# Kernel tuning notes

Hardware: AMD Instinct MI355X
Metric: run time of the kernel (lower is better)

Reference implementation:

```python
import jax, jax.numpy as jnp
import numpy as np

DIM = 128
N_ENT = 500000
N_REL = 500
GAMMA = 12.0
EPS = 1e-12  # F.normalize eps


def l2norm(x):
    n = jnp.sqrt(jnp.sum(x * x, axis=-1, keepdims=True))
    return x / jnp.maximum(n, EPS)


def setup_inputs() -> dict:
    key = jax.random.key(0)
    k1, k2, k3, k4, k5, k6 = jax.random.split(key, 6)
    B = 16384
    h = jax.random.randint(k1, (B,), 0, N_ENT)
    r = jax.random.randint(k2, (B,), 0, 2 * N_REL)
    t = jax.random.randint(k3, (B,), 0, N_ENT)
    # xavier_uniform-like init
    def xav(k, shape):
        bound = float(np.sqrt(6.0 / (shape[0] + shape[1])))
        return jax.random.uniform(k, shape, jnp.float32, -bound, bound)
    ent_w = xav(k4, (N_ENT, DIM))
    rel_w = xav(k5, (N_REL, DIM))
    mat_w = xav(k6, (N_REL, DIM * DIM))
    return {"h": h, "r": r, "t": t, "ent_w": ent_w, "rel_w": rel_w, "mat_w": mat_w}


def reference(h, r, t, ent_w, rel_w, mat_w):
    # r indexes into doubled tables: [mat; mat] and [rel; -rel]
    mat_full = jnp.concatenate([mat_w, mat_w], axis=0)          # [2R, D*D]
    rel_full = jnp.concatenate([rel_w, -rel_w], axis=0)         # [2R, D]
    mat = mat_full[r].reshape(-1, DIM, DIM)                      # [B, D, D]
    rv = l2norm(rel_full[r])                                     # [B, D]
    hv = l2norm(ent_w[h])                                        # [B, D]
    tv = l2norm(ent_w[t])                                        # [B, D]
    # _transfer: (1,D) @ (D,D) -> (D,), then L2 normalize
    hp = l2norm(jnp.einsum('bd,bde->be', hv, mat))
    tp = l2norm(jnp.einsum('bd,bde->be', tv, mat))
    dist = hp + rv - tp
    score = GAMMA - jnp.sqrt(jnp.sum(dist * dist, axis=-1))      # p=2 norm
    return score
```

## Files before the change

kernel.cpp:

```cpp
#include <hip/hip_runtime.h>

#define DIM   128
#define N_REL 500
#define GAMMA 12.0f
#define EPS   1e-12f


__global__ void k_zero(int* __restrict__ counts) {
    counts[threadIdx.x] = 0;
}

__global__ void k_hist(const int* __restrict__ r, int* __restrict__ counts, int B) {
    int i = blockIdx.x * 256 + threadIdx.x;
    if (i < B) {
        int ri = r[i];
        int mi = (ri >= N_REL) ? ri - N_REL : ri;
        atomicAdd(&counts[mi], 1);
    }
}

__global__ void k_scan(const int* __restrict__ counts,
                       int* __restrict__ offsets, int* __restrict__ cursor) {
    __shared__ int s[512];
    int tid = threadIdx.x;
    int v = counts[tid];
    s[tid] = v;
    __syncthreads();
    for (int off = 1; off < 512; off <<= 1) {
        int x = (tid >= off) ? s[tid - off] : 0;
        __syncthreads();
        s[tid] += x;
        __syncthreads();
    }
    int excl = s[tid] - v;
    offsets[tid] = excl;
    cursor[tid]  = excl;
}

__global__ void k_scatter(const int* __restrict__ r, int* __restrict__ cursor,
                          int* __restrict__ order, int B) {
    int i = blockIdx.x * 256 + threadIdx.x;
    if (i < B) {
        int ri = r[i];
        int mi = (ri >= N_REL) ? ri - N_REL : ri;
        int pos = atomicAdd(&cursor[mi], 1);
        order[pos] = i;
    }
}


__global__ __launch_bounds__(256) void k_matvec(
    const int* __restrict__ order, const int* __restrict__ offsets,
    const int* __restrict__ counts,
    const int* __restrict__ h, const int* __restrict__ t,
    const float* __restrict__ ent_w, const float* __restrict__ mat_w,
    float* __restrict__ hp_raw, float* __restrict__ tp_raw)
{
    const int rel = blockIdx.x;
    const int cnt_all = counts[rel];
    if (cnt_all == 0) return;
    const int start0 = offsets[rel];
    const int tid = threadIdx.x;
    const int eg = tid & 31;
    const int dc = tid >> 5;
    const int e128 = tid & 127;

    const float4* __restrict__ M4 = (const float4*)(mat_w + (size_t)rel * DIM * DIM);
    float4 Mreg[16];
#pragma unroll
    for (int dd = 0; dd < 16; ++dd)
        Mreg[dd] = M4[(dc * 16 + dd) * 32 + eg];

    __shared__ float sv[2][2][DIM];
    __shared__ float part[2][8][DIM];
    __shared__ int   sb[128], shi[128], sti[128];

    for (int chunk = 0; chunk < cnt_all; chunk += 128) {
        const int cc = min(128, cnt_all - chunk);

        if (tid < cc) {
            int b = order[start0 + chunk + tid];
            sb[tid]  = b;
            shi[tid] = h[b];
            sti[tid] = t[b];
        }
        __syncthreads();

        {
            int row = (tid < 128) ? shi[0] : sti[0];
            sv[0][tid >> 7][e128] = ent_w[(size_t)row * DIM + e128];
        }
        __syncthreads();

        for (int s = 0; s < cc; ++s) {
            const int cur = s & 1, nxt = cur ^ 1;

            float pre = 0.0f;
            if (s + 1 < cc) {
                int row = (tid < 128) ? shi[s + 1] : sti[s + 1];
                pre = ent_w[(size_t)row * DIM + e128];
            }

            float4 ah = make_float4(0.f, 0.f, 0.f, 0.f);
            float4 at = make_float4(0.f, 0.f, 0.f, 0.f);
#pragma unroll
            for (int dd = 0; dd < 16; ++dd) {
                const float  a = sv[cur][0][dc * 16 + dd];
                const float  c = sv[cur][1][dc * 16 + dd];
                const float4 m = Mreg[dd];
                ah.x += a * m.x; ah.y += a * m.y; ah.z += a * m.z; ah.w += a * m.w;
                at.x += c * m.x; at.y += c * m.y; at.z += c * m.z; at.w += c * m.w;
            }
            *(float4*)&part[0][dc][4 * eg] = ah;
            *(float4*)&part[1][dc][4 * eg] = at;
            __syncthreads();

            {
                const int b = sb[s];
                float v = 0.f;
                const int half = tid >> 7;
#pragma unroll
                for (int k = 0; k < 8; ++k) v += part[half][k][e128];
                float* dst = half ? tp_raw : hp_raw;
                dst[(size_t)b * DIM + e128] = v;
            }

            if (s + 1 < cc)
                sv[nxt][tid >> 7][e128] = pre;
            __syncthreads();
        }
    }
}


__device__ __forceinline__ float waveSum(float v) {
#pragma unroll
    for (int off = 32; off > 0; off >>= 1)
        v += __shfl_xor(v, off, 64);
    return v;
}

__global__ __launch_bounds__(256) void k_score(
    const int* __restrict__ r, const float* __restrict__ rel_w,
    const float* __restrict__ hp_raw, const float* __restrict__ tp_raw,
    float* __restrict__ out, int B)
{
    const int w    = threadIdx.x >> 6;
    const int lane = threadIdx.x & 63;
    const int b    = blockIdx.x * 4 + w;
    if (b >= B) return;

    const int   ri   = r[b];
    const int   mi   = (ri >= N_REL) ? ri - N_REL : ri;
    const float sign = (ri >= N_REL) ? -1.0f : 1.0f;

    const float2 hp = ((const float2*)(hp_raw + (size_t)b * DIM))[lane];
    const float2 tp = ((const float2*)(tp_raw + (size_t)b * DIM))[lane];
    const float2 rv = ((const float2*)(rel_w  + (size_t)mi * DIM))[lane];

    const float hs = waveSum(hp.x * hp.x + hp.y * hp.y);
    const float ts = waveSum(tp.x * tp.x + tp.y * tp.y);
    const float rs = waveSum(rv.x * rv.x + rv.y * rv.y);

    const float hinv = 1.0f / fmaxf(sqrtf(hs), EPS);
    const float tinv = 1.0f / fmaxf(sqrtf(ts), EPS);
    const float rinv = sign / fmaxf(sqrtf(rs), EPS);

    const float dx = hp.x * hinv + rv.x * rinv - tp.x * tinv;
    const float dy = hp.y * hinv + rv.y * rinv - tp.y * tinv;
    const float ds = waveSum(dx * dx + dy * dy);

    if (lane == 0) out[b] = GAMMA - sqrtf(ds);
}


extern "C" void kernel_launch(void* const* d_in, const int* in_sizes, int n_in,
                              void* d_out, int out_size, void* d_ws, size_t ws_size,
                              hipStream_t stream) {
    const int*   h     = (const int*)d_in[0];
    const int*   r     = (const int*)d_in[1];
    const int*   t     = (const int*)d_in[2];
    const float* ent_w = (const float*)d_in[3];
    const float* rel_w = (const float*)d_in[4];
    const float* mat_w = (const float*)d_in[5];
    float*       out   = (float*)d_out;
    const int B = in_sizes[0];

    int* counts  = (int*)d_ws;
    int* offsets = counts + 512;
    int* cursor  = counts + 1024;
    int* order   = counts + 1536;
    float* hp_raw = (float*)((char*)d_ws + (128 << 10));
    float* tp_raw = hp_raw + (size_t)B * DIM;

    k_zero   <<<1, 512, 0, stream>>>(counts);
    k_hist   <<<(B + 255) / 256, 256, 0, stream>>>(r, counts, B);
    k_scan   <<<1, 512, 0, stream>>>(counts, offsets, cursor);
    k_scatter<<<(B + 255) / 256, 256, 0, stream>>>(r, cursor, order, B);
    k_matvec <<<N_REL, 256, 0, stream>>>(order, offsets, counts, h, t,
                                         ent_w, mat_w, hp_raw, tp_raw);
    k_score  <<<(B + 3) / 4, 256, 0, stream>>>(r, rel_w, hp_raw, tp_raw, out, B);
}
```

Baseline: 367.6 us.

## Fuse scoring into matvec, merge bucketing kernels, split relations across blocks

Replaces the four bucketing kernels with one single-block kernel using shared-memory atomics and scan. It fuses the normalization and distance scoring into the matvec kernel, so the hp/tp intermediates no longer go to global memory. It also splits each relation's samples across four blocks to shorten the serial per-block loop and raise occupancy. The cost is reloading each relation matrix four times and adding an extra barrier per sample.

Result: slower. 384.4 us (+4.6%).

```diff
diff --git a/kernel.cpp b/kernel.cpp
--- a/kernel.cpp
+++ b/kernel.cpp
@@ -4,66 +4,82 @@
 #define N_REL 500
 #define GAMMA 12.0f
 #define EPS   1e-12f
+#define SPLIT 4
 
-
-__global__ void k_zero(int* __restrict__ counts) {
-    counts[threadIdx.x] = 0;
+__device__ __forceinline__ float waveSum(float v) {
+#pragma unroll
+    for (int off = 32; off > 0; off >>= 1)
+        v += __shfl_xor(v, off, 64);
+    return v;
 }
 
-__global__ void k_hist(const int* __restrict__ r, int* __restrict__ counts, int B) {
-    int i = blockIdx.x * 256 + threadIdx.x;
-    if (i < B) {
+__global__ __launch_bounds__(1024) void k_bucket(
+    const int* __restrict__ r, int B,
+    int* __restrict__ counts_g, int* __restrict__ offsets_g, int* __restrict__ order)
+{
+    __shared__ int sc[512];
+    __shared__ int sa[512];
+    __shared__ int scur[512];
+    const int tid = threadIdx.x;
+
+    if (tid < 512) sc[tid] = 0;
+    __syncthreads();
+
+    for (int i = tid; i < B; i += 1024) {
         int ri = r[i];
         int mi = (ri >= N_REL) ? ri - N_REL : ri;
-        atomicAdd(&counts[mi], 1);
+        atomicAdd(&sc[mi], 1);
     }
-}
+    __syncthreads();
 
-__global__ void k_scan(const int* __restrict__ counts,
-                       int* __restrict__ offsets, int* __restrict__ cursor) {
-    __shared__ int s[512];
-    int tid = threadIdx.x;
-    int v = counts[tid];
-    s[tid] = v;
+    if (tid < 512) sa[tid] = sc[tid];
     __syncthreads();
     for (int off = 1; off < 512; off <<= 1) {
-        int x = (tid >= off) ? s[tid - off] : 0;
+        int x = 0;
+        if (tid < 512) x = sa[tid] + ((tid >= off) ? sa[tid - off] : 0);
         __syncthreads();
-        s[tid] += x;
+        if (tid < 512) sa[tid] = x;
         __syncthreads();
     }
-    int excl = s[tid] - v;
-    offsets[tid] = excl;
-    cursor[tid]  = excl;
-}
+    if (tid < 512) {
+        int excl = sa[tid] - sc[tid];
+        offsets_g[tid] = excl;
+        counts_g[tid]  = sc[tid];
+        scur[tid]      = excl;
+    }
+    __syncthreads();
 
-__global__ void k_scatter(const int* __restrict__ r, int* __restrict__ cursor,
-                          int* __restrict__ order, int B) {
-    int i = blockIdx.x * 256 + threadIdx.x;
-    if (i < B) {
+    for (int i = tid; i < B; i += 1024) {
         int ri = r[i];
         int mi = (ri >= N_REL) ? ri - N_REL : ri;
-        int pos = atomicAdd(&cursor[mi], 1);
+        int pos = atomicAdd(&scur[mi], 1);
         order[pos] = i;
     }
 }
 
+__global__ __launch_bounds__(256) void k_main(
+    const int* __restrict__ order, const int* __restrict__ offsets_g,
+    const int* __restrict__ counts_g,
+    const int* __restrict__ h, const int* __restrict__ t, const int* __restrict__ r,
+    const float* __restrict__ ent_w, const float* __restrict__ rel_w,
+    const float* __restrict__ mat_w, float* __restrict__ out)
+{
+    const int rel = blockIdx.x / SPLIT;
+    const int sp  = blockIdx.x % SPLIT;
+    const int cnt = counts_g[rel];
+    const int lo  = (cnt * sp) / SPLIT;
+    const int hi  = (cnt * (sp + 1)) / SPLIT;
+    const int n   = hi - lo;
+    if (n <= 0) return;
+    const int base = offsets_g[rel] + lo;
 
-__global__ __launch_bounds__(256) void k_matvec(
-    const int* __restrict__ order, const int* __restrict__ offsets,
-    const int* __restrict__ counts,
-    const int* __restrict__ h, const int* __restrict__ t,
-    const float* __restrict__ ent_w, const float* __restrict__ mat_w,
-    float* __restrict__ hp_raw, float* __restrict__ tp_raw)
-{
-    const int rel = blockIdx.x;
-    const int cnt_all = counts[rel];
-    if (cnt_all == 0) return;
-    const int start0 = offsets[rel];
-    const int tid = threadIdx.x;
-    const int eg = tid & 31;
-    const int dc = tid >> 5;
-    const int e128 = tid & 127;
+    const int tid  = threadIdx.x;
+    const int eg   = tid & 31;
+    const int dc   = tid >> 5;
+    const int e    = tid & 127;
+    const int half = tid >> 7;
+    const int lane = tid & 63;
+    const int wv   = tid >> 6;
 
     const float4* __restrict__ M4 = (const float4*)(mat_w + (size_t)rel * DIM * DIM);
     float4 Mreg[16];
@@ -71,24 +87,42 @@
     for (int dd = 0; dd < 16; ++dd)
         Mreg[dd] = M4[(dc * 16 + dd) * 32 + eg];
 
+    __shared__ float srv[DIM];
     __shared__ float sv[2][2][DIM];
-    __shared__ float part[2][8][DIM];
-    __shared__ int   sb[128], shi[128], sti[128];
+    __shared__ float part[8][2][DIM];
+    __shared__ float ppv[2][DIM];
+    __shared__ float wsum[4], wsum2[4];
+    __shared__ int   sb[128], shi_a[128], sti_a[128];
+    __shared__ float ssg[128];
 
-    for (int chunk = 0; chunk < cnt_all; chunk += 128) {
-        const int cc = min(128, cnt_all - chunk);
+    {
+        float rv = (half == 0) ? rel_w[(size_t)rel * DIM + e] : 0.0f;
+        float s = waveSum(rv * rv);
+        if (lane == 0) wsum[wv] = s;
+        __syncthreads();
+        if (half == 0) {
+            float rs = wsum[0] + wsum[1];
+            srv[e] = rv / fmaxf(sqrtf(rs), EPS);
+        }
+    }
 
+    for (int chunk = 0; chunk < n; chunk += 128) {
+        const int cc = min(128, n - chunk);
+
+        __syncthreads();
         if (tid < cc) {
-            int b = order[start0 + chunk + tid];
-            sb[tid]  = b;
-            shi[tid] = h[b];
-            sti[tid] = t[b];
+            int b  = order[base + chunk + tid];
+            int ri = r[b];
+            sb[tid]    = b;
+            shi_a[tid] = h[b];
+            sti_a[tid] = t[b];
+            ssg[tid]   = (ri >= N_REL) ? -1.0f : 1.0f;
         }
         __syncthreads();
 
         {
-            int row = (tid < 128) ? shi[0] : sti[0];
-            sv[0][tid >> 7][e128] = ent_w[(size_t)row * DIM + e128];
+            int row = (half == 0) ? shi_a[0] : sti_a[0];
+            sv[0][half][e] = ent_w[(size_t)row * DIM + e];
         }
         __syncthreads();
 
@@ -97,8 +131,8 @@
 
             float pre = 0.0f;
             if (s + 1 < cc) {
-                int row = (tid < 128) ? shi[s + 1] : sti[s + 1];
-                pre = ent_w[(size_t)row * DIM + e128];
+                int row = (half == 0) ? shi_a[s + 1] : sti_a[s + 1];
+                pre = ent_w[(size_t)row * DIM + e];
             }
 
             float4 ah = make_float4(0.f, 0.f, 0.f, 0.f);
@@ -111,68 +145,36 @@
                 ah.x += a * m.x; ah.y += a * m.y; ah.z += a * m.z; ah.w += a * m.w;
                 at.x += c * m.x; at.y += c * m.y; at.z += c * m.z; at.w += c * m.w;
             }
-            *(float4*)&part[0][dc][4 * eg] = ah;
-            *(float4*)&part[1][dc][4 * eg] = at;
+            *(float4*)&part[dc][0][4 * eg] = ah;
+            *(float4*)&part[dc][1][4 * eg] = at;
             __syncthreads();
 
-            {
-                const int b = sb[s];
-                float v = 0.f;
-                const int half = tid >> 7;
+            float v = 0.f;
 #pragma unroll
-                for (int k = 0; k < 8; ++k) v += part[half][k][e128];
-                float* dst = half ? tp_raw : hp_raw;
-                dst[(size_t)b * DIM + e128] = v;
-            }
+            for (int k = 0; k < 8; ++k) v += part[k][half][e];
+            ppv[half][e] = v;
 
-            if (s + 1 < cc)
-                sv[nxt][tid >> 7][e128] = pre;
+            float sq = waveSum(v * v);
+            if (lane == 0) wsum[wv] = sq;
+
+            if (s + 1 < cc) sv[nxt][half][e] = pre;
             __syncthreads();
+
+            const float hs = wsum[0] + wsum[1];
+            const float ts = wsum[2] + wsum[3];
+            const float hinv = 1.0f / fmaxf(sqrtf(hs), EPS);
+            const float tinv = 1.0f / fmaxf(sqrtf(ts), EPS);
+
+            const float d = ppv[0][e] * hinv + ssg[s] * srv[e] - ppv[1][e] * tinv;
+            const float dsq = waveSum(d * d);
+            if (lane == 0) wsum2[wv] = dsq;
+            __syncthreads();
+
+            if (tid == 0)
+                out[sb[s]] = GAMMA - sqrtf(wsum2[0] + wsum2[1]);
         }
     }
 }
-
-
-__device__ __forceinline__ float waveSum(float v) {
-#pragma unroll
-    for (int off = 32; off > 0; off >>= 1)
-        v += __shfl_xor(v, off, 64);
-    return v;
-}
-
-__global__ __launch_bounds__(256) void k_score(
-    const int* __restrict__ r, const float* __restrict__ rel_w,
-    const float* __restrict__ hp_raw, const float* __restrict__ tp_raw,
-    float* __restrict__ out, int B)
-{
-    const int w    = threadIdx.x >> 6;
-    const int lane = threadIdx.x & 63;
-    const int b    = blockIdx.x * 4 + w;
-    if (b >= B) return;
-
-    const int   ri   = r[b];
-    const int   mi   = (ri >= N_REL) ? ri - N_REL : ri;
-    const float sign = (ri >= N_REL) ? -1.0f : 1.0f;
-
-    const float2 hp = ((const float2*)(hp_raw + (size_t)b * DIM))[lane];
-    const float2 tp = ((const float2*)(tp_raw + (size_t)b * DIM))[lane];
-    const float2 rv = ((const float2*)(rel_w  + (size_t)mi * DIM))[lane];
-
-    const float hs = waveSum(hp.x * hp.x + hp.y * hp.y);
-    const float ts = waveSum(tp.x * tp.x + tp.y * tp.y);
-    const float rs = waveSum(rv.x * rv.x + rv.y * rv.y);
-
-    const float hinv = 1.0f / fmaxf(sqrtf(hs), EPS);
-    const float tinv = 1.0f / fmaxf(sqrtf(ts), EPS);
-    const float rinv = sign / fmaxf(sqrtf(rs), EPS);
-
-    const float dx = hp.x * hinv + rv.x * rinv - tp.x * tinv;
-    const float dy = hp.y * hinv + rv.y * rinv - tp.y * tinv;
-    const float ds = waveSum(dx * dx + dy * dy);
-
-    if (lane == 0) out[b] = GAMMA - sqrtf(ds);
-}
-
 
 extern "C" void kernel_launch(void* const* d_in, const int* in_sizes, int n_in,
                               void* d_out, int out_size, void* d_ws, size_t ws_size,
@@ -188,16 +190,9 @@
 
     int* counts  = (int*)d_ws;
     int* offsets = counts + 512;
-    int* cursor  = counts + 1024;
-    int* order   = counts + 1536;
-    float* hp_raw = (float*)((char*)d_ws + (128 << 10));
-    float* tp_raw = hp_raw + (size_t)B * DIM;
+    int* order   = counts + 1024;
 
-    k_zero   <<<1, 512, 0, stream>>>(counts);
-    k_hist   <<<(B + 255) / 256, 256, 0, stream>>>(r, counts, B);
-    k_scan   <<<1, 512, 0, stream>>>(counts, offsets, cursor);
-    k_scatter<<<(B + 255) / 256, 256, 0, stream>>>(r, cursor, order, B);
-    k_matvec <<<N_REL, 256, 0, stream>>>(order, offsets, counts, h, t,
-                                         ent_w, mat_w, hp_raw, tp_raw);
-    k_score  <<<(B + 3) / 4, 256, 0, stream>>>(r, rel_w, hp_raw, tp_raw, out, B);
+    k_bucket<<<1, 1024, 0, stream>>>(r, B, counts, offsets, order);
+    k_main<<<N_REL * SPLIT, 256, 0, stream>>>(order, offsets, counts,
+                                              h, t, r, ent_w, rel_w, mat_w, out);
 }
```
